# Kernel optimization log

Measured on AMD Instinct MI355X. Metric: run time of the kernel, lower is better.

## Reference

```python
import jax, jax.numpy as jnp
import numpy as np

VOL_MIN = np.array([-40.0, -40.0, -1.0], dtype=np.float32)
VOL_MAX = np.array([40.0, 40.0, 5.4], dtype=np.float32)
VOXEL = 0.4
GRID = (200, 200, 16)          # (vol_max - vol_min) / voxel_size
SIGMA_FACTOR = 3.0
EPS = 1e-6
RMAX = 3                        # max radius given scales <= 0.4: ceil(0.4*3/0.4)=3
N_GAUSS = 16384
FEAT_DIM = 17


def setup_inputs() -> dict:
    key = jax.random.key(0)
    k1, k2, k3, k4, k5 = jax.random.split(key, 5)
    means3d = jnp.asarray(VOL_MIN) + jax.random.uniform(k1, (N_GAUSS, 3)) * jnp.asarray(VOL_MAX - VOL_MIN)
    opacities = jax.random.uniform(k2, (N_GAUSS, 1))
    scales = 0.05 + 0.35 * jax.random.uniform(k3, (N_GAUSS, 3))
    rotations = jax.random.normal(k4, (N_GAUSS, 4))
    features = jax.random.normal(k5, (N_GAUSS, FEAT_DIM))
    return {"means3d": means3d, "opacities": opacities, "scales": scales,
            "rotations": rotations, "features": features}


def _quat_to_rotmat(q):
    # q normalized; torch unbind order: r, x, y, z
    r, x, y, z = q[:, 0], q[:, 1], q[:, 2], q[:, 3]
    R = jnp.stack([
        jnp.stack([1 - 2 * (y * y + z * z), 2 * (x * y - r * z), 2 * (x * z + r * y)], -1),
        jnp.stack([2 * (x * y + r * z), 1 - 2 * (x * x + z * z), 2 * (y * z - r * x)], -1),
        jnp.stack([2 * (x * z - r * y), 2 * (y * z + r * x), 1 - 2 * (x * x + y * y)], -1),
    ], axis=1)  # [N,3,3]
    return R


def reference(means3d, opacities, scales, rotations, features):
    vol_min = jnp.asarray(VOL_MIN)
    grid = jnp.asarray(GRID, dtype=jnp.int32)

    # --- precision matrix (GaussianFormer style) ---
    q = rotations / jnp.sqrt(jnp.sum(rotations ** 2, -1, keepdims=True) + 1e-8)
    R = _quat_to_rotmat(q)
    M = scales[:, :, None] * R                       # S @ R (row-scaled)
    Cov = jnp.einsum('nki,nkj->nij', M, M)           # M^T @ M
    CovInv = jnp.linalg.inv(Cov)                     # [N,3,3]
    cxx, cyy, czz = CovInv[:, 0, 0], CovInv[:, 1, 1], CovInv[:, 2, 2]
    cxy, cyz, cxz = CovInv[:, 0, 1], CovInv[:, 1, 2], CovInv[:, 0, 2]

    radii = jnp.clip(jnp.ceil(scales.max(-1) * SIGMA_FACTOR / VOXEL), 1).astype(jnp.int32)  # [N]

    # --- fixed-window splat with per-gaussian radius mask ---
    mean_idx = jnp.floor((means3d - vol_min) / VOXEL).astype(jnp.int32)  # [N,3]
    off1 = jnp.arange(-RMAX, RMAX + 1, dtype=jnp.int32)
    oi, oj, ok = jnp.meshgrid(off1, off1, off1, indexing='ij')
    offsets = jnp.stack([oi, oj, ok], -1).reshape(-1, 3)                 # [W3,3], W3=343

    idx = mean_idx[:, None, :] + offsets[None, :, :]                     # [N,W3,3]
    centers = idx.astype(jnp.float32) * VOXEL + vol_min + 0.5 * VOXEL
    diff = means3d[:, None, :] - centers                                 # [N,W3,3]
    dx, dy, dz = diff[..., 0], diff[..., 1], diff[..., 2]
    power = (-0.5 * (cxx[:, None] * dx * dx + cyy[:, None] * dy * dy + czz[:, None] * dz * dz)
             - (cxy[:, None] * dx * dy + cyz[:, None] * dy * dz + cxz[:, None] * dx * dz))
    contrib = opacities[:, 0][:, None] * jnp.exp(power)                  # [N,W3]

    in_radius = (jnp.abs(offsets)[None, :, :] <= radii[:, None, None]).all(-1)
    in_grid = ((idx >= 0) & (idx < grid[None, None, :])).all(-1)
    contrib = jnp.where(in_radius & in_grid, contrib, 0.0)

    idx_c = jnp.clip(idx, 0, grid[None, None, :] - 1)
    flat = (idx_c[..., 0] * (GRID[1] * GRID[2]) + idx_c[..., 1] * GRID[2] + idx_c[..., 2]).reshape(-1)
    nvox = GRID[0] * GRID[1] * GRID[2]

    density = jnp.zeros((nvox,), jnp.float32).at[flat].add(contrib.reshape(-1))
    feat_contrib = (contrib[..., None] * features[:, None, :]).reshape(-1, FEAT_DIM)
    feat_acc = jnp.zeros((nvox, FEAT_DIM), jnp.float32).at[flat].add(feat_contrib)

    grid_density = density.reshape(*GRID, 1)
    grid_feats = feat_acc.reshape(*GRID, FEAT_DIM) / jnp.clip(grid_density, EPS)
    return grid_density, grid_feats
```

## Files before the change

### kernel.cpp

```cpp
#include <hip/hip_runtime.h>

#define FEAT_DIM 17
#define GX 200
#define GY 200
#define GZ 16
#define NVOX (GX * GY * GZ)
#define VOXEL 0.4f
#define EPS 1e-6f

#define TS 4
#define NTX (GX / TS)
#define NTY (GY / TS)
#define NTZ (GZ / TS)
#define NTILE (NTX * NTY * NTZ)
#define CAP 96


__global__ __launch_bounds__(256) void prep_kernel(
    const float* __restrict__ means3d,
    const float* __restrict__ opacities,
    const float* __restrict__ scales,
    const float* __restrict__ rotations,
    const float* __restrict__ features,
    float4* __restrict__ P,
    int* __restrict__ cnt,
    unsigned short* __restrict__ list,
    int N)
{
    const int g = blockIdx.x * blockDim.x + threadIdx.x;
    if (g >= N) return;

    const float mx = means3d[g * 3 + 0];
    const float my = means3d[g * 3 + 1];
    const float mz = means3d[g * 3 + 2];
    const float op = opacities[g];
    const float sx = scales[g * 3 + 0];
    const float sy = scales[g * 3 + 1];
    const float sz = scales[g * 3 + 2];
    float qr = rotations[g * 4 + 0];
    float qx = rotations[g * 4 + 1];
    float qy = rotations[g * 4 + 2];
    float qz = rotations[g * 4 + 3];

    const float qinv = 1.0f / sqrtf(qr * qr + qx * qx + qy * qy + qz * qz + 1e-8f);
    qr *= qinv; qx *= qinv; qy *= qinv; qz *= qinv;

    const float R00 = 1.0f - 2.0f * (qy * qy + qz * qz);
    const float R01 = 2.0f * (qx * qy - qr * qz);
    const float R02 = 2.0f * (qx * qz + qr * qy);
    const float R10 = 2.0f * (qx * qy + qr * qz);
    const float R11 = 1.0f - 2.0f * (qx * qx + qz * qz);
    const float R12 = 2.0f * (qy * qz - qr * qx);
    const float R20 = 2.0f * (qx * qz - qr * qy);
    const float R21 = 2.0f * (qy * qz + qr * qx);
    const float R22 = 1.0f - 2.0f * (qx * qx + qy * qy);

    const float M00 = sx * R00, M01 = sx * R01, M02 = sx * R02;
    const float M10 = sy * R10, M11 = sy * R11, M12 = sy * R12;
    const float M20 = sz * R20, M21 = sz * R21, M22 = sz * R22;

    const float C00 = M00 * M00 + M10 * M10 + M20 * M20;
    const float C01 = M00 * M01 + M10 * M11 + M20 * M21;
    const float C02 = M00 * M02 + M10 * M12 + M20 * M22;
    const float C11 = M01 * M01 + M11 * M11 + M21 * M21;
    const float C12 = M01 * M02 + M11 * M12 + M21 * M22;
    const float C22 = M02 * M02 + M12 * M12 + M22 * M22;

    const float a00 = C11 * C22 - C12 * C12;
    const float a01 = C02 * C12 - C01 * C22;
    const float a02 = C01 * C12 - C02 * C11;
    const float det = C00 * a00 + C01 * a01 + C02 * a02;
    const float idet = 1.0f / det;
    const float cxx = a00 * idet;
    const float cxy = a01 * idet;
    const float cxz = a02 * idet;
    const float cyy = (C00 * C22 - C02 * C02) * idet;
    const float cyz = (C01 * C02 - C00 * C12) * idet;
    const float czz = (C00 * C11 - C01 * C01) * idet;

    const float smax = fmaxf(sx, fmaxf(sy, sz));
    int r = (int)ceilf(smax * (3.0f / VOXEL));
    if (r < 1) r = 1;
    if (r > 3) r = 3;

    const int cx = (int)floorf((mx + 40.0f) / VOXEL);
    const int cy = (int)floorf((my + 40.0f) / VOXEL);
    const int cz = (int)floorf((mz + 1.0f) / VOXEL);

    const int pk = (cx & 255) | ((cy & 255) << 8) | ((cz & 63) << 16) | (r << 22);

    float4* p = P + ((size_t)g << 3);
    const float* ft = features + (size_t)g * FEAT_DIM;
    p[0] = make_float4(mx, my, mz, op);
    p[1] = make_float4(cxx, cyy, czz, __int_as_float(pk));
    p[2] = make_float4(cxy, cyz, cxz, ft[16]);
    p[3] = make_float4(ft[0], ft[1], ft[2], ft[3]);
    p[4] = make_float4(ft[4], ft[5], ft[6], ft[7]);
    p[5] = make_float4(ft[8], ft[9], ft[10], ft[11]);
    p[6] = make_float4(ft[12], ft[13], ft[14], ft[15]);

    const int txl = max(0, cx - r) / TS, txh = min(GX - 1, cx + r) / TS;
    const int tyl = max(0, cy - r) / TS, tyh = min(GY - 1, cy + r) / TS;
    const int tzl = max(0, cz - r) / TS, tzh = min(GZ - 1, cz + r) / TS;
    for (int tx = txl; tx <= txh; ++tx)
        for (int ty = tyl; ty <= tyh; ++ty)
            for (int tz = tzl; tz <= tzh; ++tz) {
                const int t = (tx * NTY + ty) * NTZ + tz;
                const int pos = atomicAdd(&cnt[t], 1);
                if (pos < CAP) list[(size_t)t * CAP + pos] = (unsigned short)g;
            }
}

__global__ __launch_bounds__(256) void gather_kernel(
    const float4* __restrict__ P,
    const int* __restrict__ cnt,
    const unsigned int* __restrict__ list32,
    float* __restrict__ out)
{
    const int wid = threadIdx.x >> 6;
    const int lane = threadIdx.x & 63;
    const int t = blockIdx.x * 4 + wid;

    const int tz = t & (NTZ - 1);
    const int ty = (t >> 2) % NTY;
    const int tx = (t >> 2) / NTY;

    const int lz = lane & 3;
    const int ly = (lane >> 2) & 3;
    const int lx = lane >> 4;
    const int ix = tx * TS + lx;
    const int iy = ty * TS + ly;
    const int iz = tz * TS + lz;

    const float vx = (float)ix * VOXEL - 40.0f + 0.5f * VOXEL;
    const float vy = (float)iy * VOXEL - 40.0f + 0.5f * VOXEL;
    const float vz = (float)iz * VOXEL - 1.0f + 0.5f * VOXEL;

    const int st = __builtin_amdgcn_readfirstlane(t);
    const int ncand = min(cnt[st], CAP);

    const unsigned int vpair = list32[(size_t)st * (CAP / 2) + min(lane, CAP / 2 - 1)];

    float dacc = 0.0f;
    float facc[FEAT_DIM];
#pragma unroll
    for (int f = 0; f < FEAT_DIM; ++f) facc[f] = 0.0f;

    if (ncand > 0) {
        unsigned int pr0 = __builtin_amdgcn_readlane(vpair, 0);
        int sg = (int)(pr0 & 0xffffu);
        const float4* ap = P + ((size_t)sg << 3);
        float4 a0 = ap[0], a1 = ap[1], a2 = ap[2], a3 = ap[3],
               a4 = ap[4], a5 = ap[5], a6 = ap[6];

        for (int c = 0; c < ncand; ++c) {
            const int cn = min(c + 1, ncand - 1);
            const unsigned int pairn = __builtin_amdgcn_readlane(vpair, cn >> 1);
            const int sgn = (int)((cn & 1) ? (pairn >> 16) : (pairn & 0xffffu));
            const float4* bp = P + ((size_t)sgn << 3);
            const float4 b0 = bp[0], b1 = bp[1], b2 = bp[2], b3 = bp[3],
                         b4 = bp[4], b5 = bp[5], b6 = bp[6];

            const int pk = __float_as_int(a1.w);
            const int cx = pk & 255;
            const int cy = (pk >> 8) & 255;
            const int cz = (pk >> 16) & 63;
            const int r  = (pk >> 22) & 3;
            const bool inr = (abs(ix - cx) <= r) && (abs(iy - cy) <= r) && (abs(iz - cz) <= r);

            const float dx = a0.x - vx;
            const float dy = a0.y - vy;
            const float dz = a0.z - vz;
            const float power = -0.5f * (a1.x * dx * dx + a1.y * dy * dy + a1.z * dz * dz)
                                - (a2.x * dx * dy + a2.y * dy * dz + a2.z * dx * dz);
            const float w = inr ? a0.w * __expf(power) : 0.0f;

            dacc += w;
            facc[0]  += w * a3.x;  facc[1]  += w * a3.y;
            facc[2]  += w * a3.z;  facc[3]  += w * a3.w;
            facc[4]  += w * a4.x;  facc[5]  += w * a4.y;
            facc[6]  += w * a4.z;  facc[7]  += w * a4.w;
            facc[8]  += w * a5.x;  facc[9]  += w * a5.y;
            facc[10] += w * a5.z;  facc[11] += w * a5.w;
            facc[12] += w * a6.x;  facc[13] += w * a6.y;
            facc[14] += w * a6.z;  facc[15] += w * a6.w;
            facc[16] += w * a2.w;

            a0 = b0; a1 = b1; a2 = b2; a3 = b3; a4 = b4; a5 = b5; a6 = b6;
        }
    }

    const int flat = ix * (GY * GZ) + iy * GZ + iz;
    out[flat] = dacc;

    const float inv = 1.0f / fmaxf(dacc, EPS);
    float* fo = out + NVOX + (size_t)flat * FEAT_DIM;
#pragma unroll
    for (int f = 0; f < FEAT_DIM; ++f) fo[f] = facc[f] * inv;
}

extern "C" void kernel_launch(void* const* d_in, const int* in_sizes, int n_in,
                              void* d_out, int out_size, void* d_ws, size_t ws_size,
                              hipStream_t stream) {
    const float* means3d   = (const float*)d_in[0];
    const float* opacities = (const float*)d_in[1];
    const float* scales    = (const float*)d_in[2];
    const float* rotations = (const float*)d_in[3];
    const float* features  = (const float*)d_in[4];

    const int n_gauss = in_sizes[0] / 3;

    char* ws = (char*)d_ws;
    float4* P = (float4*)ws;
    size_t off = ((size_t)n_gauss << 3) * sizeof(float4);
    int* cnt = (int*)(ws + off);
    off += (size_t)NTILE * sizeof(int);
    unsigned short* list = (unsigned short*)(ws + off);

    hipMemsetAsync(cnt, 0, (size_t)NTILE * sizeof(int), stream);

    prep_kernel<<<dim3((n_gauss + 255) / 256), dim3(256), 0, stream>>>(
        means3d, opacities, scales, rotations, features, P, cnt, list, n_gauss);

    gather_kernel<<<dim3(NTILE / 4), dim3(256), 0, stream>>>(
        P, cnt, (const unsigned int*)list, (float*)d_out);
}
```

Before: 126.5 us.

## Process candidate pairs per iteration, batch tile atomics, shrink prep blocks

The gather loop now handles two gaussians per iteration taken from one packed 32-bit list entry. It drops the software-prefetch double buffer and issues both gaussians' loads together, accumulating into float2 pairs, which is meant to raise memory-level parallelism and cut readlane overhead. The prep kernel unrolls its tile binning into 27 predicated atomics issued before any list writes, so the atomic latencies overlap, and it now launches 64-thread blocks. This costs more registers in both kernels, and the odd last candidate is masked with a validity flag.

```diff
diff --git a/kernel.cpp b/kernel.cpp
--- a/kernel.cpp
+++ b/kernel.cpp
@@ -16,7 +16,7 @@
 #define CAP 96
 
 
-__global__ __launch_bounds__(256) void prep_kernel(
+__global__ __launch_bounds__(64) void prep_kernel(
     const float* __restrict__ means3d,
     const float* __restrict__ opacities,
     const float* __restrict__ scales,
@@ -102,13 +102,24 @@
     const int txl = max(0, cx - r) / TS, txh = min(GX - 1, cx + r) / TS;
     const int tyl = max(0, cy - r) / TS, tyh = min(GY - 1, cy + r) / TS;
     const int tzl = max(0, cz - r) / TS, tzh = min(GZ - 1, cz + r) / TS;
-    for (int tx = txl; tx <= txh; ++tx)
-        for (int ty = tyl; ty <= tyh; ++ty)
-            for (int tz = tzl; tz <= tzh; ++tz) {
-                const int t = (tx * NTY + ty) * NTZ + tz;
-                const int pos = atomicAdd(&cnt[t], 1);
-                if (pos < CAP) list[(size_t)t * CAP + pos] = (unsigned short)g;
-            }
+
+    int ts_[27];
+    int ps_[27];
+#pragma unroll
+    for (int s = 0; s < 27; ++s) {
+        const int tx = txl + s / 9;
+        const int ty = tyl + (s / 3) % 3;
+        const int tz = tzl + s % 3;
+        const bool v = (tx <= txh) && (ty <= tyh) && (tz <= tzh);
+        const int t = (tx * NTY + ty) * NTZ + tz;
+        ts_[s] = v ? t : -1;
+        ps_[s] = v ? atomicAdd(&cnt[t], 1) : CAP;
+    }
+#pragma unroll
+    for (int s = 0; s < 27; ++s) {
+        if (ts_[s] >= 0 && ps_[s] < CAP)
+            list[(size_t)ts_[s] * CAP + ps_[s]] = (unsigned short)g;
+    }
 }
 
 __global__ __launch_bounds__(256) void gather_kernel(
@@ -139,64 +150,72 @@
     const int st = __builtin_amdgcn_readfirstlane(t);
     const int ncand = min(cnt[st], CAP);
 
-    const unsigned int vpair = list32[(size_t)st * (CAP / 2) + min(lane, CAP / 2 - 1)];
-
-    float dacc = 0.0f;
-    float facc[FEAT_DIM];
+    const unsigned int vpair =
+        list32[(size_t)st * (CAP / 2) + min(lane, CAP / 2 - 1)];
+
+    float2 facc2[9];
 #pragma unroll
-    for (int f = 0; f < FEAT_DIM; ++f) facc[f] = 0.0f;
-
-    if (ncand > 0) {
-        unsigned int pr0 = __builtin_amdgcn_readlane(vpair, 0);
-        int sg = (int)(pr0 & 0xffffu);
-        const float4* ap = P + ((size_t)sg << 3);
-        float4 a0 = ap[0], a1 = ap[1], a2 = ap[2], a3 = ap[3],
-               a4 = ap[4], a5 = ap[5], a6 = ap[6];
-
-        for (int c = 0; c < ncand; ++c) {
-            const int cn = min(c + 1, ncand - 1);
-            const unsigned int pairn = __builtin_amdgcn_readlane(vpair, cn >> 1);
-            const int sgn = (int)((cn & 1) ? (pairn >> 16) : (pairn & 0xffffu));
-            const float4* bp = P + ((size_t)sgn << 3);
-            const float4 b0 = bp[0], b1 = bp[1], b2 = bp[2], b3 = bp[3],
-                         b4 = bp[4], b5 = bp[5], b6 = bp[6];
-
-            const int pk = __float_as_int(a1.w);
-            const int cx = pk & 255;
-            const int cy = (pk >> 8) & 255;
-            const int cz = (pk >> 16) & 63;
-            const int r  = (pk >> 22) & 3;
-            const bool inr = (abs(ix - cx) <= r) && (abs(iy - cy) <= r) && (abs(iz - cz) <= r);
-
-            const float dx = a0.x - vx;
-            const float dy = a0.y - vy;
-            const float dz = a0.z - vz;
-            const float power = -0.5f * (a1.x * dx * dx + a1.y * dy * dy + a1.z * dz * dz)
-                                - (a2.x * dx * dy + a2.y * dy * dz + a2.z * dx * dz);
-            const float w = inr ? a0.w * __expf(power) : 0.0f;
-
-            dacc += w;
-            facc[0]  += w * a3.x;  facc[1]  += w * a3.y;
-            facc[2]  += w * a3.z;  facc[3]  += w * a3.w;
-            facc[4]  += w * a4.x;  facc[5]  += w * a4.y;
-            facc[6]  += w * a4.z;  facc[7]  += w * a4.w;
-            facc[8]  += w * a5.x;  facc[9]  += w * a5.y;
-            facc[10] += w * a5.z;  facc[11] += w * a5.w;
-            facc[12] += w * a6.x;  facc[13] += w * a6.y;
-            facc[14] += w * a6.z;  facc[15] += w * a6.w;
-            facc[16] += w * a2.w;
-
-            a0 = b0; a1 = b1; a2 = b2; a3 = b3; a4 = b4; a5 = b5; a6 = b6;
-        }
+    for (int j = 0; j < 9; ++j) facc2[j] = make_float2(0.0f, 0.0f);
+
+    for (int c = 0; c < ncand; c += 2) {
+        const unsigned int pair =
+            (unsigned int)__builtin_amdgcn_readlane((int)vpair, c >> 1);
+        const int sgA = (int)(pair & 0xffffu);
+        const int sgB = (int)(pair >> 16);
+        const bool bval = (c + 1) < ncand;
+
+        const float4* pa = P + ((size_t)sgA << 3);
+        const float4* pb = P + ((size_t)sgB << 3);
+        const float4 a0 = pa[0], a1 = pa[1], a2 = pa[2], a3 = pa[3],
+                     a4 = pa[4], a5 = pa[5], a6 = pa[6];
+        const float4 b0 = pb[0], b1 = pb[1], b2 = pb[2], b3 = pb[3],
+                     b4 = pb[4], b5 = pb[5], b6 = pb[6];
+
+        const int pkA = __float_as_int(a1.w);
+        const bool inrA = (abs(ix - (pkA & 255)) <= ((pkA >> 22) & 3)) &&
+                          (abs(iy - ((pkA >> 8) & 255)) <= ((pkA >> 22) & 3)) &&
+                          (abs(iz - ((pkA >> 16) & 63)) <= ((pkA >> 22) & 3));
+        const float dxA = a0.x - vx, dyA = a0.y - vy, dzA = a0.z - vz;
+        const float powA = -0.5f * (a1.x * dxA * dxA + a1.y * dyA * dyA + a1.z * dzA * dzA)
+                           - (a2.x * dxA * dyA + a2.y * dyA * dzA + a2.z * dxA * dzA);
+        const float wA = inrA ? a0.w * __expf(powA) : 0.0f;
+
+        const int pkB = __float_as_int(b1.w);
+        const bool inrB = bval &&
+                          (abs(ix - (pkB & 255)) <= ((pkB >> 22) & 3)) &&
+                          (abs(iy - ((pkB >> 8) & 255)) <= ((pkB >> 22) & 3)) &&
+                          (abs(iz - ((pkB >> 16) & 63)) <= ((pkB >> 22) & 3));
+        const float dxB = b0.x - vx, dyB = b0.y - vy, dzB = b0.z - vz;
+        const float powB = -0.5f * (b1.x * dxB * dxB + b1.y * dyB * dyB + b1.z * dzB * dzB)
+                           - (b2.x * dxB * dyB + b2.y * dyB * dzB + b2.z * dxB * dzB);
+        const float wB = inrB ? b0.w * __expf(powB) : 0.0f;
+
+        facc2[0].x += wA * a3.x + wB * b3.x;  facc2[0].y += wA * a3.y + wB * b3.y;
+        facc2[1].x += wA * a3.z + wB * b3.z;  facc2[1].y += wA * a3.w + wB * b3.w;
+        facc2[2].x += wA * a4.x + wB * b4.x;  facc2[2].y += wA * a4.y + wB * b4.y;
+        facc2[3].x += wA * a4.z + wB * b4.z;  facc2[3].y += wA * a4.w + wB * b4.w;
+        facc2[4].x += wA * a5.x + wB * b5.x;  facc2[4].y += wA * a5.y + wB * b5.y;
+        facc2[5].x += wA * a5.z + wB * b5.z;  facc2[5].y += wA * a5.w + wB * b5.w;
+        facc2[6].x += wA * a6.x + wB * b6.x;  facc2[6].y += wA * a6.y + wB * b6.y;
+        facc2[7].x += wA * a6.z + wB * b6.z;  facc2[7].y += wA * a6.w + wB * b6.w;
+        facc2[8].x += wA * a2.w + wB * b2.w;  facc2[8].y += wA + wB;
     }
 
+    const float dacc = facc2[8].y;
     const int flat = ix * (GY * GZ) + iy * GZ + iz;
     out[flat] = dacc;
 
     const float inv = 1.0f / fmaxf(dacc, EPS);
     float* fo = out + NVOX + (size_t)flat * FEAT_DIM;
-#pragma unroll
-    for (int f = 0; f < FEAT_DIM; ++f) fo[f] = facc[f] * inv;
+    fo[0]  = facc2[0].x * inv;  fo[1]  = facc2[0].y * inv;
+    fo[2]  = facc2[1].x * inv;  fo[3]  = facc2[1].y * inv;
+    fo[4]  = facc2[2].x * inv;  fo[5]  = facc2[2].y * inv;
+    fo[6]  = facc2[3].x * inv;  fo[7]  = facc2[3].y * inv;
+    fo[8]  = facc2[4].x * inv;  fo[9]  = facc2[4].y * inv;
+    fo[10] = facc2[5].x * inv;  fo[11] = facc2[5].y * inv;
+    fo[12] = facc2[6].x * inv;  fo[13] = facc2[6].y * inv;
+    fo[14] = facc2[7].x * inv;  fo[15] = facc2[7].y * inv;
+    fo[16] = facc2[8].x * inv;
 }
 
 extern "C" void kernel_launch(void* const* d_in, const int* in_sizes, int n_in,
@@ -219,7 +238,7 @@
 
     hipMemsetAsync(cnt, 0, (size_t)NTILE * sizeof(int), stream);
 
-    prep_kernel<<<dim3((n_gauss + 255) / 256), dim3(256), 0, stream>>>(
+    prep_kernel<<<dim3((n_gauss + 63) / 64), dim3(64), 0, stream>>>(
         means3d, opacities, scales, rotations, features, P, cnt, list, n_gauss);
 
     gather_kernel<<<dim3(NTILE / 4), dim3(256), 0, stream>>>(
```

Measured after the change: 121.3 us. -4.2%, faster.
